# Performance work log

Hardware: AMD Instinct MI355X
Metric: run time of the kernel (lower is better)

Reference implementation:

```python
import jax, jax.numpy as jnp
import numpy as np


def setup_inputs() -> dict:
    key = jax.random.key(0)
    kx, kq, kk, kv = jax.random.split(key, 4)
    d_model, d_head = 1024, 64
    x = jax.random.normal(kx, (4, 4096, d_model), dtype=jnp.float32)
    scale = 1.0 / np.sqrt(d_model)
    Wq = jax.random.normal(kq, (d_model, d_head), dtype=jnp.float32) * scale
    Wk = jax.random.normal(kk, (d_model, d_head), dtype=jnp.float32) * scale
    Wv = jax.random.normal(kv, (d_model, d_head), dtype=jnp.float32) * scale
    return {"x": x, "Wq": Wq, "Wk": Wk, "Wv": Wv}


def reference(x, Wq, Wk, Wv):
    # x: [B, S, D]; Wq/Wk/Wv: [D, H]
    d_head = Wq.shape[-1]
    Q = jnp.einsum('bsd,dh->bsh', x, Wq)
    K = jnp.einsum('bsd,dh->bsh', x, Wk)
    V = jnp.einsum('bsd,dh->bsh', x, Wv)
    scores = jnp.einsum('bqh,bkh->bqk', Q, K) / jnp.sqrt(jnp.float32(d_head))
    S = x.shape[1]
    causal = jnp.tril(jnp.ones((S, S), dtype=bool))  # [S, S]
    scores = jnp.where(causal, scores, -jnp.inf)
    weights = jax.nn.softmax(scores, axis=-1)  # [B, S, S]
    return jnp.einsum('bqk,bkh->bqh', weights, V)
```

## Files before the change

kernel.cpp:

```cpp
#include <hip/hip_runtime.h>

#define D_MODEL 1024
#define D_HEAD  64
#define SEQ     4096
#define BATCH   4
#define M_TOT   (BATCH * SEQ)
#define LOG2E   1.44269504088896f
#define MFIX_L2 17.3123404906676f
#define CHUNK   8

typedef __bf16 bf16;
typedef bf16  bf16x8 __attribute__((ext_vector_type(8)));
typedef float f32x4  __attribute__((ext_vector_type(4)));

#define MFMA(a, b, c) __builtin_amdgcn_mfma_f32_16x16x32_bf16(a, b, c, 0, 0, 0)

#define QKV_OFF  0
#define OBUF_OFF 6291456
#define LBUF_OFF 10485760
#define WT_OFF   10551296
#define VT_OFF   10944512

__global__ void prep_kernel(const float* __restrict__ Wq, const float* __restrict__ Wk,
                            const float* __restrict__ Wv, bf16* __restrict__ Wt,
                            float4* __restrict__ zp, int n4)
{
    const int bx = blockIdx.x;
    const int t  = threadIdx.x;
    if (bx < 48) {
        __shared__ bf16 tr[64][72];
        const int wm = bx >> 4, kt = bx & 15, k0 = kt * 64;
        const float* W = (wm == 0) ? Wq : (wm == 1) ? Wk : Wv;
        const int kr = t >> 2, nb = (t & 3) * 16;
        #pragma unroll
        for (int j = 0; j < 4; j++) {
            float4 wrow = *(const float4*)(W + (size_t)(k0 + kr) * D_HEAD + nb + j * 4);
            tr[nb + j * 4 + 0][kr] = (bf16)wrow.x;
            tr[nb + j * 4 + 1][kr] = (bf16)wrow.y;
            tr[nb + j * 4 + 2][kr] = (bf16)wrow.z;
            tr[nb + j * 4 + 3][kr] = (bf16)wrow.w;
        }
        __syncthreads();
        const int n = t >> 2, kc = (t & 3) * 8;
        bf16* dst = Wt + (size_t)(wm * 64 + n) * D_MODEL + k0;
        #pragma unroll
        for (int h = 0; h < 2; h++) {
            bf16x8 v;
            #pragma unroll
            for (int j = 0; j < 8; j++) v[j] = tr[n][kc + h * 32 + j];
            *(bf16x8*)(dst + kc + h * 32) = v;
        }
    } else {
        int i = (bx - 48) * 256 + t;
        if (i < n4) zp[i] = float4{0.f, 0.f, 0.f, 0.f};
    }
}

#define XP 40

__global__ __launch_bounds__(512) void proj_kernel(
    const float* __restrict__ x, const bf16* __restrict__ Wt,
    bf16* __restrict__ qkv)
{
    __shared__ __align__(16) bf16 xs[2][2][64][XP];
    __shared__ __align__(16) bf16 ws[2][2][192][XP];
    __shared__ float red[64][193];

    const int t    = threadIdx.x;
    const int w    = t >> 6;
    const int g    = w >> 2;
    const int nw   = w & 3;
    const int lane = t & 63;
    const int quad = lane >> 4;
    const int l15  = lane & 15;
    const int row0 = blockIdx.x * 64;
    const int kb   = g * 512;

    const int tg   = t & 255;
    const int xrow = tg >> 2, xkq = (tg & 3) * 8;

    const float* xg = x + (size_t)(row0 + xrow) * D_MODEL + kb + xkq;

    f32x4 acc[12] = {};

    float4 xa, xb;
    bf16x8 wtv[3];

    auto load_regs = [&](int c) {
        xa = *(const float4*)(xg + c * 32);
        xb = *(const float4*)(xg + c * 32 + 4);
        #pragma unroll
        for (int it = 0; it < 3; it++) {
            int id = tg + it * 256, n = id >> 2, kk8 = (id & 3) * 8;
            wtv[it] = *(const bf16x8*)(Wt + (size_t)n * D_MODEL + kb + c * 32 + kk8);
        }
    };
    auto store_lds = [&](int p) {
        bf16x8 xv;
        xv[0] = (bf16)xa.x; xv[1] = (bf16)xa.y; xv[2] = (bf16)xa.z; xv[3] = (bf16)xa.w;
        xv[4] = (bf16)xb.x; xv[5] = (bf16)xb.y; xv[6] = (bf16)xb.z; xv[7] = (bf16)xb.w;
        *(bf16x8*)&xs[p][g][xrow][xkq] = xv;
        #pragma unroll
        for (int it = 0; it < 3; it++) {
            int id = tg + it * 256, n = id >> 2, kk8 = (id & 3) * 8;
            *(bf16x8*)&ws[p][g][n][kk8] = wtv[it];
        }
    };

    load_regs(0);
    store_lds(0);
    load_regs(1);
    __syncthreads();

    int p = 0;
    for (int c = 0; c < 16; c++) {
        bf16x8 af[4], bfr[3];
        #pragma unroll
        for (int rg = 0; rg < 4; rg++)
            af[rg] = *(bf16x8*)&xs[p][g][rg * 16 + l15][quad * 8];
        #pragma unroll
        for (int j = 0; j < 3; j++)
            bfr[j] = *(bf16x8*)&ws[p][g][nw * 48 + j * 16 + l15][quad * 8];
        #pragma unroll
        for (int rg = 0; rg < 4; rg++)
            #pragma unroll
            for (int j = 0; j < 3; j++)
                acc[rg * 3 + j] = MFMA(af[rg], bfr[j], acc[rg * 3 + j]);

        if (c + 1 < 16) {
            store_lds(p ^ 1);
            if (c + 2 < 16) load_regs(c + 2);
        }
        __syncthreads();
        p ^= 1;
    }

    if (g == 1) {
        #pragma unroll
        for (int rg = 0; rg < 4; rg++)
            #pragma unroll
            for (int j = 0; j < 3; j++)
                #pragma unroll
                for (int r = 0; r < 4; r++)
                    red[rg * 16 + quad * 4 + r][nw * 48 + j * 16 + l15] =
                        acc[rg * 3 + j][r];
    }
    __syncthreads();
    if (g == 0) {
        #pragma unroll
        for (int rg = 0; rg < 4; rg++)
            #pragma unroll
            for (int j = 0; j < 3; j++) {
                const int col = nw * 48 + j * 16 + l15;
                const int wm = col >> 6, h = col & 63;
                const float sc = (wm == 0) ? 0.125f : 1.0f;
                bf16* outp = qkv + (size_t)wm * M_TOT * D_HEAD;
                #pragma unroll
                for (int r = 0; r < 4; r++) {
                    const int row = rg * 16 + quad * 4 + r;
                    float s = acc[rg * 3 + j][r] + red[row][col];
                    outp[(size_t)(row0 + row) * D_HEAD + h] = (bf16)(s * sc);
                }
            }
    }
}

__global__ void vtrans_kernel(const bf16* __restrict__ qkv, bf16* __restrict__ vt)
{
    __shared__ bf16 trs[64][72];
    const bf16* Vsec = qkv + (size_t)2 * M_TOT * D_HEAD;
    const int t  = threadIdx.x;
    const int m0 = blockIdx.x * 64;
    const int b  = m0 >> 12, s0 = m0 & (SEQ - 1);

    #pragma unroll
    for (int half = 0; half < 2; half++) {
        const int ml = (t >> 3) + half * 32, hc = t & 7;
        bf16x8 v = *(const bf16x8*)(Vsec + (size_t)(m0 + ml) * D_HEAD + hc * 8);
        #pragma unroll
        for (int j = 0; j < 8; j++) trs[hc * 8 + j][ml] = v[j];
    }
    __syncthreads();
    #pragma unroll
    for (int half = 0; half < 2; half++) {
        const int hl = (t >> 3) + half * 32, sc = t & 7;
        bf16x8 v;
        #pragma unroll
        for (int j = 0; j < 8; j++) v[j] = trs[hl][sc * 8 + j];
        *(bf16x8*)(vt + ((size_t)b * D_HEAD + hl) * SEQ + s0 + sc * 8) = v;
    }
}

#define TS 72

__global__ __launch_bounds__(256) void attn_kernel(
    const bf16* __restrict__ qkv, const bf16* __restrict__ vt,
    float* __restrict__ o_buf, float* __restrict__ l_buf)
{
    const int i = blockIdx.x;
    const int c = blockIdx.y;
    const int b = blockIdx.z;
    const int ntiles = i + 1;
    const int tile0  = c * CHUNK;
    if (tile0 >= ntiles) return;
    const int tile1 = min(tile0 + CHUNK, ntiles);

    __shared__ __align__(16) bf16 Ks[2][64][TS];
    __shared__ __align__(16) bf16 Vs[2][64][TS];
    __shared__ __align__(16) bf16 Ps[4][16][TS];

    const bf16* Q = qkv;
    const bf16* K = qkv + (size_t)M_TOT * D_HEAD;

    const int t    = threadIdx.x;
    const int wv   = t >> 6;
    const int lane = t & 63;
    const int quad = lane >> 4;
    const int l15  = lane & 15;
    const int qb   = i * 64;
    const size_t base  = (size_t)b * SEQ * D_HEAD;
    const bf16* vtb = vt + (size_t)b * D_HEAD * SEQ;

    bf16x8 qf0, qf1;
    {
        const bf16* qr = Q + base + (size_t)(qb + wv * 16 + l15) * D_HEAD;
        qf0 = *(const bf16x8*)(qr + quad * 8);
        qf1 = *(const bf16x8*)(qr + 32 + quad * 8);
    }

    f32x4 o[4] = {};
    float l_r[4] = {};
    const int qw0 = qb + wv * 16;

    const int dr  = t >> 2;
    const int kq8 = (t & 3) * 8;

    bf16x8 kr0, kr1, vr0, vr1;
    auto load_kv = [&](int tile) {
        const bf16* kp = K + base + (size_t)(tile * 64 + dr) * D_HEAD;
        kr0 = *(const bf16x8*)(kp + kq8);
        kr1 = *(const bf16x8*)(kp + kq8 + 32);
        const bf16* vp = vtb + (size_t)dr * SEQ + tile * 64;
        vr0 = *(const bf16x8*)(vp + kq8);
        vr1 = *(const bf16x8*)(vp + kq8 + 32);
    };
    auto store_kv = [&](int p) {
        *(bf16x8*)&Ks[p][dr][kq8]      = kr0;
        *(bf16x8*)&Ks[p][dr][kq8 + 32] = kr1;
        *(bf16x8*)&Vs[p][dr][kq8]      = vr0;
        *(bf16x8*)&Vs[p][dr][kq8 + 32] = vr1;
    };

    load_kv(tile0);
    store_kv(0);
    if (tile0 + 1 < tile1) load_kv(tile0 + 1);
    __syncthreads();

    int p = 0;
    for (int tile = tile0; tile < tile1; tile++) {
        const int kk0 = tile * 64;

        f32x4 sc4[4];
        #pragma unroll
        for (int kt = 0; kt < 4; kt++) {
            f32x4 z = {};
            z = MFMA(qf0, *(bf16x8*)&Ks[p][kt * 16 + l15][quad * 8],      z);
            z = MFMA(qf1, *(bf16x8*)&Ks[p][kt * 16 + l15][32 + quad * 8], z);
            sc4[kt] = z;
        }

        if (tile == i) {
            #pragma unroll
            for (int r = 0; r < 4; r++) {
                #pragma unroll
                for (int kt = 0; kt < 4; kt++) {
                    float s = sc4[kt][r];
                    if (kk0 + kt * 16 + l15 > qw0 + quad * 4 + r)
                        s = -1e30f;
                    float pe = __builtin_amdgcn_exp2f(fmaf(s, LOG2E, -MFIX_L2));
                    l_r[r] += pe;
                    Ps[wv][quad * 4 + r][kt * 16 + l15] = (bf16)pe;
                }
            }
        } else {
            #pragma unroll
            for (int r = 0; r < 4; r++) {
                #pragma unroll
                for (int kt = 0; kt < 4; kt++) {
                    float pe = __builtin_amdgcn_exp2f(
                        fmaf(sc4[kt][r], LOG2E, -MFIX_L2));
                    l_r[r] += pe;
                    Ps[wv][quad * 4 + r][kt * 16 + l15] = (bf16)pe;
                }
            }
        }
        asm volatile("s_waitcnt lgkmcnt(0)" ::: "memory");

        #pragma unroll
        for (int c2 = 0; c2 < 2; c2++) {
            bf16x8 pa = *(bf16x8*)&Ps[wv][l15][c2 * 32 + quad * 8];
            #pragma unroll
            for (int t4 = 0; t4 < 4; t4++) {
                bf16x8 vb = *(bf16x8*)&Vs[p][t4 * 16 + l15][c2 * 32 + quad * 8];
                o[t4] = MFMA(pa, vb, o[t4]);
            }
        }

        if (tile + 1 < tile1) {
            store_kv(p ^ 1);
            if (tile + 2 < tile1) load_kv(tile + 2);
            __syncthreads();
        }
        p ^= 1;
    }

    const int mrow0 = b * SEQ + qw0;
    #pragma unroll
    for (int r = 0; r < 4; r++) {
        float ls = l_r[r];
        #pragma unroll
        for (int sh = 1; sh < 16; sh <<= 1)
            ls += __shfl_xor(ls, sh, 64);
        if (l15 == 0)
            atomicAdd(&l_buf[mrow0 + quad * 4 + r], ls);
        const size_t orow = (size_t)(mrow0 + quad * 4 + r) * D_HEAD;
        #pragma unroll
        for (int t4 = 0; t4 < 4; t4++)
            atomicAdd(&o_buf[orow + t4 * 16 + l15], o[t4][r]);
    }
}

__global__ void norm_kernel(const float4* __restrict__ o_buf,
                            const float* __restrict__ l_buf,
                            float4* __restrict__ out)
{
    int gid = blockIdx.x * 256 + threadIdx.x;
    int m = gid >> 4;
    float inv = 1.0f / l_buf[m];
    float4 v = o_buf[gid];
    out[gid] = float4{v.x * inv, v.y * inv, v.z * inv, v.w * inv};
}

extern "C" void kernel_launch(void* const* d_in, const int* in_sizes, int n_in,
                              void* d_out, int out_size, void* d_ws, size_t ws_size,
                              hipStream_t stream) {
    const float* x  = (const float*)d_in[0];
    const float* Wq = (const float*)d_in[1];
    const float* Wk = (const float*)d_in[2];
    const float* Wv = (const float*)d_in[3];

    bf16*  qkv   = (bf16*)((char*)d_ws + QKV_OFF);
    float* o_buf = (float*)((char*)d_ws + OBUF_OFF);
    float* l_buf = (float*)((char*)d_ws + LBUF_OFF);
    bf16*  Wt    = (bf16*)((char*)d_ws + WT_OFF);
    bf16*  vt    = (bf16*)((char*)d_ws + VT_OFF);

    const int zero4 = (M_TOT * 65) / 4;
    const int zblocks = (zero4 + 255) / 256;
    prep_kernel<<<48 + zblocks, 256, 0, stream>>>(Wq, Wk, Wv, Wt,
                                                  (float4*)o_buf, zero4);
    proj_kernel<<<M_TOT / 64, 512, 0, stream>>>(x, Wt, qkv);
    vtrans_kernel<<<M_TOT / 64, 256, 0, stream>>>(qkv, vt);
    attn_kernel<<<dim3(SEQ / 64, SEQ / 64 / CHUNK, BATCH), 256, 0, stream>>>(
        qkv, vt, o_buf, l_buf);
    norm_kernel<<<M_TOT * 16 / 256, 256, 0, stream>>>((const float4*)o_buf, l_buf,
                                                      (float4*)d_out);
}
```

Before: 150.8 us.

## Fuse V transpose into projection and keep P in registers in attention

The projection kernel now writes V directly in transposed layout, which removes the separate vtrans kernel launch and its extra pass over V. The attention kernel swaps the MFMA operands so that the score tile comes out transposed. The probabilities are then passed between lanes with shuffles instead of being staged through shared memory. K/V shared tiles use an XOR swizzle instead of padding, setprio hints are placed around the MFMA blocks, and launch bounds now request 4 blocks per CU. The risks are extra shuffle instructions and the correctness of the new lane mapping.

```diff
diff --git a/kernel.cpp b/kernel.cpp
--- a/kernel.cpp
+++ b/kernel.cpp
@@ -11,6 +11,7 @@
 
 typedef __bf16 bf16;
 typedef bf16  bf16x8 __attribute__((ext_vector_type(8)));
+typedef bf16  bf16x4v __attribute__((ext_vector_type(4)));
 typedef float f32x4  __attribute__((ext_vector_type(4)));
 
 #define MFMA(a, b, c) __builtin_amdgcn_mfma_f32_16x16x32_bf16(a, b, c, 0, 0, 0)
@@ -60,7 +61,7 @@
 
 __global__ __launch_bounds__(512) void proj_kernel(
     const float* __restrict__ x, const bf16* __restrict__ Wt,
-    bf16* __restrict__ qkv)
+    bf16* __restrict__ qkv, bf16* __restrict__ vt)
 {
     __shared__ __align__(16) bf16 xs[2][2][64][XP];
     __shared__ __align__(16) bf16 ws[2][2][192][XP];
@@ -147,53 +148,37 @@
     }
     __syncthreads();
     if (g == 0) {
+        const int bb = row0 >> 12, s0 = row0 & (SEQ - 1);
         #pragma unroll
         for (int rg = 0; rg < 4; rg++)
             #pragma unroll
             for (int j = 0; j < 3; j++) {
                 const int col = nw * 48 + j * 16 + l15;
                 const int wm = col >> 6, h = col & 63;
-                const float sc = (wm == 0) ? 0.125f : 1.0f;
-                bf16* outp = qkv + (size_t)wm * M_TOT * D_HEAD;
-                #pragma unroll
-                for (int r = 0; r < 4; r++) {
-                    const int row = rg * 16 + quad * 4 + r;
-                    float s = acc[rg * 3 + j][r] + red[row][col];
-                    outp[(size_t)(row0 + row) * D_HEAD + h] = (bf16)(s * sc);
+                if (wm == 2) {
+                    bf16x4v vv;
+                    #pragma unroll
+                    for (int r = 0; r < 4; r++) {
+                        const int row = rg * 16 + quad * 4 + r;
+                        vv[r] = (bf16)(acc[rg * 3 + j][r] + red[row][col]);
+                    }
+                    *(bf16x4v*)(vt + ((size_t)bb * D_HEAD + h) * SEQ +
+                                s0 + rg * 16 + quad * 4) = vv;
+                } else {
+                    const float sc = (wm == 0) ? 0.125f : 1.0f;
+                    bf16* outp = qkv + (size_t)wm * M_TOT * D_HEAD;
+                    #pragma unroll
+                    for (int r = 0; r < 4; r++) {
+                        const int row = rg * 16 + quad * 4 + r;
+                        float s = acc[rg * 3 + j][r] + red[row][col];
+                        outp[(size_t)(row0 + row) * D_HEAD + h] = (bf16)(s * sc);
+                    }
                 }
             }
     }
 }
 
-__global__ void vtrans_kernel(const bf16* __restrict__ qkv, bf16* __restrict__ vt)
-{
-    __shared__ bf16 trs[64][72];
-    const bf16* Vsec = qkv + (size_t)2 * M_TOT * D_HEAD;
-    const int t  = threadIdx.x;
-    const int m0 = blockIdx.x * 64;
-    const int b  = m0 >> 12, s0 = m0 & (SEQ - 1);
-
-    #pragma unroll
-    for (int half = 0; half < 2; half++) {
-        const int ml = (t >> 3) + half * 32, hc = t & 7;
-        bf16x8 v = *(const bf16x8*)(Vsec + (size_t)(m0 + ml) * D_HEAD + hc * 8);
-        #pragma unroll
-        for (int j = 0; j < 8; j++) trs[hc * 8 + j][ml] = v[j];
-    }
-    __syncthreads();
-    #pragma unroll
-    for (int half = 0; half < 2; half++) {
-        const int hl = (t >> 3) + half * 32, sc = t & 7;
-        bf16x8 v;
-        #pragma unroll
-        for (int j = 0; j < 8; j++) v[j] = trs[hl][sc * 8 + j];
-        *(bf16x8*)(vt + ((size_t)b * D_HEAD + hl) * SEQ + s0 + sc * 8) = v;
-    }
-}
-
-#define TS 72
-
-__global__ __launch_bounds__(256) void attn_kernel(
+__global__ __launch_bounds__(256, 4) void attn_kernel(
     const bf16* __restrict__ qkv, const bf16* __restrict__ vt,
     float* __restrict__ o_buf, float* __restrict__ l_buf)
 {
@@ -205,9 +190,12 @@
     if (tile0 >= ntiles) return;
     const int tile1 = min(tile0 + CHUNK, ntiles);
 
-    __shared__ __align__(16) bf16 Ks[2][64][TS];
-    __shared__ __align__(16) bf16 Vs[2][64][TS];
-    __shared__ __align__(16) bf16 Ps[4][16][TS];
+    __shared__ __align__(16) char KsB[2 * 64 * 128];
+    __shared__ __align__(16) char VsB[2 * 64 * 128];
+
+    auto kaddr = [](char* base, int pp, int row, int colb) -> void* {
+        return base + pp * 8192 + row * 128 + (colb ^ ((row & 7) << 4));
+    };
 
     const bf16* Q = qkv;
     const bf16* K = qkv + (size_t)M_TOT * D_HEAD;
@@ -229,26 +217,26 @@
     }
 
     f32x4 o[4] = {};
-    float l_r[4] = {};
+    float lsum = 0.f;
     const int qw0 = qb + wv * 16;
 
     const int dr  = t >> 2;
-    const int kq8 = (t & 3) * 8;
+    const int cb  = (t & 3) * 16;
 
     bf16x8 kr0, kr1, vr0, vr1;
     auto load_kv = [&](int tile) {
         const bf16* kp = K + base + (size_t)(tile * 64 + dr) * D_HEAD;
-        kr0 = *(const bf16x8*)(kp + kq8);
-        kr1 = *(const bf16x8*)(kp + kq8 + 32);
+        kr0 = *(const bf16x8*)(kp + (cb >> 1));
+        kr1 = *(const bf16x8*)(kp + (cb >> 1) + 32);
         const bf16* vp = vtb + (size_t)dr * SEQ + tile * 64;
-        vr0 = *(const bf16x8*)(vp + kq8);
-        vr1 = *(const bf16x8*)(vp + kq8 + 32);
-    };
-    auto store_kv = [&](int p) {
-        *(bf16x8*)&Ks[p][dr][kq8]      = kr0;
-        *(bf16x8*)&Ks[p][dr][kq8 + 32] = kr1;
-        *(bf16x8*)&Vs[p][dr][kq8]      = vr0;
-        *(bf16x8*)&Vs[p][dr][kq8 + 32] = vr1;
+        vr0 = *(const bf16x8*)(vp + (cb >> 1));
+        vr1 = *(const bf16x8*)(vp + (cb >> 1) + 32);
+    };
+    auto store_kv = [&](int pp) {
+        *(bf16x8*)kaddr(KsB, pp, dr, cb)      = kr0;
+        *(bf16x8*)kaddr(KsB, pp, dr, cb + 64) = kr1;
+        *(bf16x8*)kaddr(VsB, pp, dr, cb)      = vr0;
+        *(bf16x8*)kaddr(VsB, pp, dr, cb + 64) = vr1;
     };
 
     load_kv(tile0);
@@ -261,49 +249,78 @@
         const int kk0 = tile * 64;
 
         f32x4 sc4[4];
+        __builtin_amdgcn_s_setprio(1);
         #pragma unroll
         for (int kt = 0; kt < 4; kt++) {
             f32x4 z = {};
-            z = MFMA(qf0, *(bf16x8*)&Ks[p][kt * 16 + l15][quad * 8],      z);
-            z = MFMA(qf1, *(bf16x8*)&Ks[p][kt * 16 + l15][32 + quad * 8], z);
+            z = MFMA(*(bf16x8*)kaddr(KsB, p, kt * 16 + l15, quad * 16),      qf0, z);
+            z = MFMA(*(bf16x8*)kaddr(KsB, p, kt * 16 + l15, 64 + quad * 16), qf1, z);
             sc4[kt] = z;
         }
-
+        __builtin_amdgcn_s_setprio(0);
+
+        bf16 ph[4][4];
         if (tile == i) {
             #pragma unroll
-            for (int r = 0; r < 4; r++) {
+            for (int kt = 0; kt < 4; kt++)
                 #pragma unroll
-                for (int kt = 0; kt < 4; kt++) {
+                for (int r = 0; r < 4; r++) {
                     float s = sc4[kt][r];
-                    if (kk0 + kt * 16 + l15 > qw0 + quad * 4 + r)
+                    if (kk0 + kt * 16 + quad * 4 + r > qw0 + l15)
                         s = -1e30f;
                     float pe = __builtin_amdgcn_exp2f(fmaf(s, LOG2E, -MFIX_L2));
-                    l_r[r] += pe;
-                    Ps[wv][quad * 4 + r][kt * 16 + l15] = (bf16)pe;
+                    lsum += pe;
+                    ph[kt][r] = (bf16)pe;
                 }
-            }
         } else {
             #pragma unroll
-            for (int r = 0; r < 4; r++) {
+            for (int kt = 0; kt < 4; kt++)
                 #pragma unroll
-                for (int kt = 0; kt < 4; kt++) {
+                for (int r = 0; r < 4; r++) {
                     float pe = __builtin_amdgcn_exp2f(
                         fmaf(sc4[kt][r], LOG2E, -MFIX_L2));
-                    l_r[r] += pe;
-                    Ps[wv][quad * 4 + r][kt * 16 + l15] = (bf16)pe;
+                    lsum += pe;
+                    ph[kt][r] = (bf16)pe;
                 }
-            }
-        }
-        asm volatile("s_waitcnt lgkmcnt(0)" ::: "memory");
+        }
+
+        unsigned pku[4][2];
+        #pragma unroll
+        for (int kt = 0; kt < 4; kt++) {
+            __builtin_memcpy(&pku[kt][0], &ph[kt][0], 4);
+            __builtin_memcpy(&pku[kt][1], &ph[kt][2], 4);
+        }
+
+        const int srcA = l15 + ((lane & 16) ? 32 : 0);
+        const int srcB = srcA + 16;
+        const bool hi  = (lane & 32) != 0;
 
         #pragma unroll
         for (int c2 = 0; c2 < 2; c2++) {
-            bf16x8 pa = *(bf16x8*)&Ps[wv][l15][c2 * 32 + quad * 8];
+            unsigned xA0 = __shfl((int)pku[2 * c2][0],     srcA);
+            unsigned xA1 = __shfl((int)pku[2 * c2][1],     srcA);
+            unsigned yA0 = __shfl((int)pku[2 * c2 + 1][0], srcA);
+            unsigned yA1 = __shfl((int)pku[2 * c2 + 1][1], srcA);
+            unsigned xB0 = __shfl((int)pku[2 * c2][0],     srcB);
+            unsigned xB1 = __shfl((int)pku[2 * c2][1],     srcB);
+            unsigned yB0 = __shfl((int)pku[2 * c2 + 1][0], srcB);
+            unsigned yB1 = __shfl((int)pku[2 * c2 + 1][1], srcB);
+            unsigned fr[4];
+            fr[0] = hi ? yA0 : xA0;
+            fr[1] = hi ? yA1 : xA1;
+            fr[2] = hi ? yB0 : xB0;
+            fr[3] = hi ? yB1 : xB1;
+            bf16x8 pa;
+            __builtin_memcpy(&pa, fr, 16);
+
+            __builtin_amdgcn_s_setprio(1);
             #pragma unroll
             for (int t4 = 0; t4 < 4; t4++) {
-                bf16x8 vb = *(bf16x8*)&Vs[p][t4 * 16 + l15][c2 * 32 + quad * 8];
+                bf16x8 vb = *(bf16x8*)kaddr(VsB, p, t4 * 16 + l15,
+                                            c2 * 64 + quad * 16);
                 o[t4] = MFMA(pa, vb, o[t4]);
             }
+            __builtin_amdgcn_s_setprio(0);
         }
 
         if (tile + 1 < tile1) {
@@ -315,14 +332,12 @@
     }
 
     const int mrow0 = b * SEQ + qw0;
+    lsum += __shfl_xor(lsum, 16, 64);
+    lsum += __shfl_xor(lsum, 32, 64);
+    if (lane < 16)
+        atomicAdd(&l_buf[mrow0 + l15], lsum);
     #pragma unroll
     for (int r = 0; r < 4; r++) {
-        float ls = l_r[r];
-        #pragma unroll
-        for (int sh = 1; sh < 16; sh <<= 1)
-            ls += __shfl_xor(ls, sh, 64);
-        if (l15 == 0)
-            atomicAdd(&l_buf[mrow0 + quad * 4 + r], ls);
         const size_t orow = (size_t)(mrow0 + quad * 4 + r) * D_HEAD;
         #pragma unroll
         for (int t4 = 0; t4 < 4; t4++)
@@ -359,8 +374,7 @@
     const int zblocks = (zero4 + 255) / 256;
     prep_kernel<<<48 + zblocks, 256, 0, stream>>>(Wq, Wk, Wv, Wt,
                                                   (float4*)o_buf, zero4);
-    proj_kernel<<<M_TOT / 64, 512, 0, stream>>>(x, Wt, qkv);
-    vtrans_kernel<<<M_TOT / 64, 256, 0, stream>>>(qkv, vt);
+    proj_kernel<<<M_TOT / 64, 512, 0, stream>>>(x, Wt, qkv, vt);
     attn_kernel<<<dim3(SEQ / 64, SEQ / 64 / CHUNK, BATCH), 256, 0, stream>>>(
         qkv, vt, o_buf, l_buf);
     norm_kernel<<<M_TOT * 16 / 256, 256, 0, stream>>>((const float4*)o_buf, l_buf,
```

Result: faster. 147.8 us (-2.0%).
